# Kernel optimization log

Hardware: AMD Instinct MI355X
Metric: run time of the kernel (lower is better)

Reference implementation:

```python
import jax, jax.numpy as jnp
import numpy as np

N_BLOCKS = 12   # grid rows == cols
D = 256         # per-block feature size (small -> memory-bound)
BATCH = 8192    # samples per block

# Deterministic block-sparse pattern: block (i, j) is active iff (i - j) % 3 == 0.
_mask = np.array([[(i - j) % 3 == 0 for j in range(N_BLOCKS)] for i in range(N_BLOCKS)])
_I, _J = np.nonzero(_mask)  # 48 active blocks
N_ACTIVE = _I.shape[0]


def setup_inputs() -> dict:
    key = jax.random.key(0)
    k1, k2, k3 = jax.random.split(key, 3)
    X = jax.random.normal(k1, (N_BLOCKS, BATCH, D), dtype=jnp.float32)
    # One Linear(D, D) per active block: weight [K, D_in, D_out], bias [K, D_out]
    W = jax.random.normal(k2, (N_ACTIVE, D, D), dtype=jnp.float32) / np.sqrt(D).astype(np.float32)
    b = jax.random.normal(k3, (N_ACTIVE, D), dtype=jnp.float32) * 0.01
    i_idx = jnp.asarray(_I, dtype=jnp.int32)  # output-row index of each active block
    j_idx = jnpim if False else jnp.asarray(_J, dtype=jnp.int32)  # input-col index of each active block
    return {"X": X, "W": W, "b": b, "i_idx": i_idx, "j_idx": j_idx}


def reference(X, W, b, i_idx, j_idx):
    # Gather the input block feeding each active sub-module: [K, BATCH, D]
    Xg = X[j_idx]
    # Apply each block's Linear in one batched contraction: [K, BATCH, D]
    h = jnp.einsum('kbi,kio->kbo', Xg, W) + b[:, None, :]
    # Sum block outputs into their output rows (the '+' combiner / safe_sum):
    # rows with no active block get an all-zero output, matching the zero-vector semantics.
    y = jax.ops.segment_sum(h, i_idx, num_segments=N_BLOCKS)  # [N_BLOCKS, BATCH, D]
    return y
```

## Files before the change

### kernel.cpp

```cpp
#include <hip/hip_runtime.h>

#define N_BLOCKS 12
#define D 256
#define BATCH 8192

typedef __attribute__((ext_vector_type(8))) short bf16x8;
typedef __attribute__((ext_vector_type(4))) float f32x4;

__device__ __forceinline__ unsigned short f2bf(float f) {
  unsigned int u = __float_as_uint(f);
  u += 0x7fffu + ((u >> 16) & 1u);
  return (unsigned short)(u >> 16);
}

__device__ __forceinline__ void gld16(const unsigned short* g, unsigned short* l) {
  __builtin_amdgcn_global_load_lds(
      (const __attribute__((address_space(1))) unsigned int*)g,
      (__attribute__((address_space(3))) unsigned int*)l,
      16, 0, 0);
}

__global__ void cvt_x(const float* __restrict__ X, unsigned short* __restrict__ Xb) {
  const long long t = (long long)blockIdx.x * 256 + threadIdx.x;
  const long long base = t * 8;
  const float4 v0 = *(const float4*)(X + base);
  const float4 v1 = *(const float4*)(X + base + 4);
  uint4 r;
  r.x = (unsigned)f2bf(v0.x) | ((unsigned)f2bf(v0.y) << 16);
  r.y = (unsigned)f2bf(v0.z) | ((unsigned)f2bf(v0.w) << 16);
  r.z = (unsigned)f2bf(v1.x) | ((unsigned)f2bf(v1.y) << 16);
  r.w = (unsigned)f2bf(v1.z) | ((unsigned)f2bf(v1.w) << 16);
  *(uint4*)(Xb + base) = r;
}

__global__ void cvt_w(const float* __restrict__ W, unsigned short* __restrict__ Wt) {
  __shared__ unsigned short tile[32][33];
  const int k  = blockIdx.x >> 6;
  const int t  = blockIdx.x & 63;
  const int ti = t >> 3;
  const int tj = t & 7;
  const float* Wk = W + (long long)k * D * D;
  unsigned short* Wtk = Wt + (long long)k * D * D;
  const int lx = threadIdx.x & 31, ly = threadIdx.x >> 5;
  #pragma unroll
  for (int r = 0; r < 4; ++r) {
    const int i = ti * 32 + ly + r * 8;
    const int o = tj * 32 + lx;
    tile[ly + r * 8][lx] = f2bf(Wk[i * D + o]);
  }
  __syncthreads();
  #pragma unroll
  for (int r = 0; r < 4; ++r) {
    const int o = tj * 32 + ly + r * 8;
    const int i = ti * 32 + lx;
    Wtk[o * D + i] = tile[lx][ly + r * 8];
  }
}

__launch_bounds__(512, 4)
__global__ void bs_gemm(const unsigned short* __restrict__ Xb,
                        const unsigned short* __restrict__ Wt,
                        const float* __restrict__ bias,
                        const int* __restrict__ i_idx,
                        const int* __restrict__ j_idx,
                        int nact,
                        float* __restrict__ Y) {
  __shared__ unsigned short lds[5 * 8192];

  const int bid = blockIdx.x;
  const int x   = bid & 7;
  const int r   = bid >> 3;
  const int i   = r >> 4;
  const int rem = r & 15;
  const int bm  = x * 8 + (rem >> 1);
  const int bn  = rem & 1;

  int ks0 = 0, ks1 = 0, ks2 = 0, ks3 = 0, js0 = 0, js1 = 0, js2 = 0, js3 = 0, nk = 0;
  for (int k = 0; k < nact; ++k) {
    if (i_idx[k] == i) {
      const int j = j_idx[k];
      if      (nk == 0) { ks0 = k; js0 = j; }
      else if (nk == 1) { ks1 = k; js1 = j; }
      else if (nk == 2) { ks2 = k; js2 = j; }
      else              { ks3 = k; js3 = j; }
      ++nk;
    }
  }
#define JS(t) ((t) == 0 ? js0 : (t) == 1 ? js1 : (t) == 2 ? js2 : js3)
#define KS(t) ((t) == 0 ? ks0 : (t) == 1 ? ks1 : (t) == 2 ? ks2 : ks3)

  const int tid  = threadIdx.x;
  const int wave = tid >> 6;
  const int lane = tid & 63;
  const int wm   = wave >> 1;
  const int wn   = wave & 1;
  const int q    = lane >> 4;
  const int l15  = lane & 15;

  const int g_off = (tid >> 2) * D + (tid & 3) * 8;
  const int dA = tid * 8;
  const int dB = 4096 + tid * 8;

  const int aR0 = (wm * 32 +  0 + l15) * 64 + q * 16;
  const int aR1 = (wm * 32 + 16 + l15) * 64 + q * 16;
  const int bB  = 8192;
  const int bR0 = bB + (wn * 64 +  0 + l15) * 64 + q * 16;
  const int bR1 = bB + (wn * 64 + 16 + l15) * 64 + q * 16;
  const int bR2 = bB + (wn * 64 + 32 + l15) * 64 + q * 16;
  const int bR3 = bB + (wn * 64 + 48 + l15) * 64 + q * 16;

  auto STAGE = [&](int st) {
    const int t  = st >> 3;
    const int kk = st & 7;
    unsigned short* sl = lds + (st % 5) * 8192;
    const unsigned short* As =
        Xb + ((long long)JS(t) * BATCH + bm * 128) * D + kk * 32 + g_off;
    const unsigned short* Bs =
        Wt + ((long long)KS(t) * D + bn * 128) * D + kk * 32 + g_off;
    gld16(As, sl + dA);
    gld16(Bs, sl + dB);
  };

  f32x4 acc[2][4] = {};

  STAGE(0); STAGE(1); STAGE(2); STAGE(3);

  #pragma unroll
  for (int kt = 0; kt < 32; ++kt) {
    if      (kt <= 28) asm volatile("s_waitcnt vmcnt(6)" ::: "memory");
    else if (kt == 29) asm volatile("s_waitcnt vmcnt(4)" ::: "memory");
    else if (kt == 30) asm volatile("s_waitcnt vmcnt(2)" ::: "memory");
    else               asm volatile("s_waitcnt vmcnt(0)" ::: "memory");
    __builtin_amdgcn_s_barrier();
    __builtin_amdgcn_sched_barrier(0);

    const char* sb = (const char*)lds + (kt % 5) * 16384;
    bf16x8 aF[2], bF[4];
    aF[0] = *(const bf16x8*)(sb + aR0);
    aF[1] = *(const bf16x8*)(sb + aR1);
    bF[0] = *(const bf16x8*)(sb + bR0);
    bF[1] = *(const bf16x8*)(sb + bR1);
    bF[2] = *(const bf16x8*)(sb + bR2);
    bF[3] = *(const bf16x8*)(sb + bR3);

    if (kt < 28) STAGE(kt + 4);

    asm volatile("s_waitcnt lgkmcnt(0)" ::: "memory");
    __builtin_amdgcn_sched_barrier(0);

    __builtin_amdgcn_s_setprio(1);
    #pragma unroll
    for (int mf = 0; mf < 2; ++mf)
      #pragma unroll
      for (int nf = 0; nf < 4; ++nf)
        acc[mf][nf] = __builtin_amdgcn_mfma_f32_16x16x32_bf16(
            aF[mf], bF[nf], acc[mf][nf], 0, 0, 0);
    __builtin_amdgcn_s_setprio(0);
  }

  float* Yb = Y + (long long)i * BATCH * D;
  const int m0 = bm * 128 + wm * 32 + q * 4;
  const int n0 = bn * 128 + wn * 64 + l15;
  float bsum[4];
  #pragma unroll
  for (int nf = 0; nf < 4; ++nf) {
    float s = 0.f;
    for (int t = 0; t < nk; ++t) s += bias[KS(t) * D + n0 + nf * 16];
    bsum[nf] = s;
  }
  #pragma unroll
  for (int nf = 0; nf < 4; ++nf) {
    #pragma unroll
    for (int mf = 0; mf < 2; ++mf)
      #pragma unroll
      for (int r2 = 0; r2 < 4; ++r2)
        Yb[(long long)(m0 + mf * 16 + r2) * D + (n0 + nf * 16)] =
            acc[mf][nf][r2] + bsum[nf];
  }
#undef JS
#undef KS
}

extern "C" void kernel_launch(void* const* d_in, const int* in_sizes, int n_in,
                              void* d_out, int out_size, void* d_ws, size_t ws_size,
                              hipStream_t stream) {
  const float* X = (const float*)d_in[0];
  const float* W = (const float*)d_in[1];
  const float* b = (const float*)d_in[2];
  const int* i_idx = (const int*)d_in[3];
  const int* j_idx = (const int*)d_in[4];
  float* Y = (float*)d_out;
  const int nact = in_sizes[3];

  unsigned short* Xb = (unsigned short*)d_ws;
  unsigned short* Wt = (unsigned short*)((char*)d_ws + (size_t)N_BLOCKS * BATCH * D * 2);

  cvt_x<<<(N_BLOCKS * BATCH * D) / (256 * 8), 256, 0, stream>>>(X, Xb);
  cvt_w<<<nact * 64, 256, 0, stream>>>(W, Wt);
  bs_gemm<<<N_BLOCKS * 64 * 2, 512, 0, stream>>>(Xb, Wt, b, i_idx, j_idx, nact, Y);
}
```

Baseline: 260.1 us.

## Keep full weight slab in LDS and stream X tiles directly from global

The GEMM kernel used to stage both the X tile and the weight tile through a 5-deep LDS pipeline. It now preloads the whole 64-column weight slice for all four K-blocks (128 KB, with XOR swizzling) into LDS once. Each wave then reads its 64-row X fragments straight from global memory into registers, with no LDS staging and no per-step barriers. Tiles grow to 512 rows by 64 columns, the grid is remapped per XCD, and occupancy drops to 2 blocks. The risk is exposed global-load latency for A, since there is no software prefetch, plus a large LDS footprint limiting residency.

```diff
diff --git a/kernel.cpp b/kernel.cpp
--- a/kernel.cpp
+++ b/kernel.cpp
@@ -57,7 +57,7 @@
   }
 }
 
-__launch_bounds__(512, 4)
+__launch_bounds__(512, 2)
 __global__ void bs_gemm(const unsigned short* __restrict__ Xb,
                         const unsigned short* __restrict__ Wt,
                         const float* __restrict__ bias,
@@ -65,15 +65,16 @@
                         const int* __restrict__ j_idx,
                         int nact,
                         float* __restrict__ Y) {
-  __shared__ unsigned short lds[5 * 8192];
+  __shared__ unsigned short sB[65536];
 
   const int bid = blockIdx.x;
-  const int x   = bid & 7;
-  const int r   = bid >> 3;
-  const int i   = r >> 4;
-  const int rem = r & 15;
-  const int bm  = x * 8 + (rem >> 1);
-  const int bn  = rem & 1;
+  const int xcd = bid & 7;
+  const int loc = bid >> 3;
+  const int bn  = loc & 3;
+  const int pm  = loc >> 2;
+  const int P   = xcd * 24 + pm;
+  const int i   = P >> 4;
+  const int bm  = P & 15;
 
   int ks0 = 0, ks1 = 0, ks2 = 0, ks3 = 0, js0 = 0, js1 = 0, js2 = 0, js3 = 0, nk = 0;
   for (int k = 0; k < nact; ++k) {
@@ -92,65 +93,44 @@
   const int tid  = threadIdx.x;
   const int wave = tid >> 6;
   const int lane = tid & 63;
-  const int wm   = wave >> 1;
-  const int wn   = wave & 1;
   const int q    = lane >> 4;
   const int l15  = lane & 15;
 
-  const int g_off = (tid >> 2) * D + (tid & 3) * 8;
-  const int dA = tid * 8;
-  const int dB = 4096 + tid * 8;
+  #pragma unroll
+  for (int it = 0; it < 16; ++it) {
+    const int L  = it * 8192 + tid * 16;
+    const int n  = L >> 11;
+    const int cc = ((L >> 4) & 127) ^ (n & 7);
+    const int t  = cc >> 5;
+    const unsigned short* src = Wt + (long long)KS(t) * (D * D)
+                              + (long long)(bn * 64 + n) * D + (cc & 31) * 8;
+    gld16(src, sB + (L >> 1));
+  }
+  __syncthreads();
 
-  const int aR0 = (wm * 32 +  0 + l15) * 64 + q * 16;
-  const int aR1 = (wm * 32 + 16 + l15) * 64 + q * 16;
-  const int bB  = 8192;
-  const int bR0 = bB + (wn * 64 +  0 + l15) * 64 + q * 16;
-  const int bR1 = bB + (wn * 64 + 16 + l15) * 64 + q * 16;
-  const int bR2 = bB + (wn * 64 + 32 + l15) * 64 + q * 16;
-  const int bR3 = bB + (wn * 64 + 48 + l15) * 64 + q * 16;
+  const int bcon = l15 * 2048 + ((q ^ (l15 & 3)) << 4) + (((l15 >> 2) & 1) << 6);
+  const long long arow = ((long long)bm * 512 + wave * 64 + l15) * D + q * 8;
 
-  auto STAGE = [&](int st) {
-    const int t  = st >> 3;
-    const int kk = st & 7;
-    unsigned short* sl = lds + (st % 5) * 8192;
-    const unsigned short* As =
-        Xb + ((long long)JS(t) * BATCH + bm * 128) * D + kk * 32 + g_off;
-    const unsigned short* Bs =
-        Wt + ((long long)KS(t) * D + bn * 128) * D + kk * 32 + g_off;
-    gld16(As, sl + dA);
-    gld16(Bs, sl + dB);
-  };
-
-  f32x4 acc[2][4] = {};
-
-  STAGE(0); STAGE(1); STAGE(2); STAGE(3);
+  f32x4 acc[4][4] = {};
 
   #pragma unroll
   for (int kt = 0; kt < 32; ++kt) {
-    if      (kt <= 28) asm volatile("s_waitcnt vmcnt(6)" ::: "memory");
-    else if (kt == 29) asm volatile("s_waitcnt vmcnt(4)" ::: "memory");
-    else if (kt == 30) asm volatile("s_waitcnt vmcnt(2)" ::: "memory");
-    else               asm volatile("s_waitcnt vmcnt(0)" ::: "memory");
-    __builtin_amdgcn_s_barrier();
-    __builtin_amdgcn_sched_barrier(0);
-
-    const char* sb = (const char*)lds + (kt % 5) * 16384;
-    bf16x8 aF[2], bF[4];
-    aF[0] = *(const bf16x8*)(sb + aR0);
-    aF[1] = *(const bf16x8*)(sb + aR1);
-    bF[0] = *(const bf16x8*)(sb + bR0);
-    bF[1] = *(const bf16x8*)(sb + bR1);
-    bF[2] = *(const bf16x8*)(sb + bR2);
-    bF[3] = *(const bf16x8*)(sb + bR3);
-
-    if (kt < 28) STAGE(kt + 4);
-
-    asm volatile("s_waitcnt lgkmcnt(0)" ::: "memory");
-    __builtin_amdgcn_sched_barrier(0);
+    const int t  = kt >> 3;
+    const int kk = kt & 7;
+    const unsigned short* Ab =
+        Xb + (long long)JS(t) * (BATCH * (long long)D) + arow + kk * 32;
+    bf16x8 aF[4], bF[4];
+    #pragma unroll
+    for (int mf = 0; mf < 4; ++mf)
+      aF[mf] = *(const bf16x8*)(Ab + mf * (16 * D));
+    const int bb = (bcon ^ ((kt & 1) << 6)) + ((kt >> 1) << 7);
+    #pragma unroll
+    for (int nf = 0; nf < 4; ++nf)
+      bF[nf] = *(const bf16x8*)((const char*)sB + bb + nf * 32768);
 
     __builtin_amdgcn_s_setprio(1);
     #pragma unroll
-    for (int mf = 0; mf < 2; ++mf)
+    for (int mf = 0; mf < 4; ++mf)
       #pragma unroll
       for (int nf = 0; nf < 4; ++nf)
         acc[mf][nf] = __builtin_amdgcn_mfma_f32_16x16x32_bf16(
@@ -159,8 +139,8 @@
   }
 
   float* Yb = Y + (long long)i * BATCH * D;
-  const int m0 = bm * 128 + wm * 32 + q * 4;
-  const int n0 = bn * 128 + wn * 64 + l15;
+  const int m0 = bm * 512 + wave * 64 + q * 4;
+  const int n0 = bn * 64 + l15;
   float bsum[4];
   #pragma unroll
   for (int nf = 0; nf < 4; ++nf) {
@@ -171,7 +151,7 @@
   #pragma unroll
   for (int nf = 0; nf < 4; ++nf) {
     #pragma unroll
-    for (int mf = 0; mf < 2; ++mf)
+    for (int mf = 0; mf < 4; ++mf)
       #pragma unroll
       for (int r2 = 0; r2 < 4; ++r2)
         Yb[(long long)(m0 + mf * 16 + r2) * D + (n0 + nf * 16)] =
@@ -197,5 +177,5 @@
 
   cvt_x<<<(N_BLOCKS * BATCH * D) / (256 * 8), 256, 0, stream>>>(X, Xb);
   cvt_w<<<nact * 64, 256, 0, stream>>>(W, Wt);
-  bs_gemm<<<N_BLOCKS * 64 * 2, 512, 0, stream>>>(Xb, Wt, b, i_idx, j_idx, nact, Y);
+  bs_gemm<<<768, 512, 0, stream>>>(Xb, Wt, b, i_idx, j_idx, nact, Y);
 }
```

Measured after the change: 314.9 us. 21.0% more time.
